# Optimization experiments

Hardware: AMD Instinct MI355X
Metric: run time of the kernel (lower is better)

The kernel has to match this reference:

```python
import jax, jax.numpy as jnp
import numpy as np

N_USERS = 200000
N_ITEMS = 100000
N_EDGES = 4800000
EMBED_DIM = 64
N_LAYERS = 3
BATCH = 16384


def setup_inputs() -> dict:
    key = jax.random.key(0)
    ks = jax.random.split(key, 7)
    N = N_USERS + N_ITEMS
    user_embed = jax.random.normal(ks[0], (N_USERS, EMBED_DIM), dtype=jnp.float32)
    item_embed = jax.random.normal(ks[1], (N_ITEMS, EMBED_DIM), dtype=jnp.float32)
    edge_src = jax.random.randint(ks[2], (N_EDGES,), 0, N, dtype=jnp.int32)
    edge_dst = jax.random.randint(ks[3], (N_EDGES,), 0, N, dtype=jnp.int32)
    # stands in for symmetric normalization 1/sqrt(deg_i*deg_j), avg degree ~16
    edge_val = jax.random.uniform(ks[4], (N_EDGES,), dtype=jnp.float32) * 0.0625
    users = jax.random.randint(ks[5], (BATCH,), 0, N_USERS, dtype=jnp.int32)
    items = jax.random.randint(ks[6], (BATCH,), 0, N_ITEMS, dtype=jnp.int32)
    return {"user_embed": user_embed, "item_embed": item_embed,
            "edge_src": edge_src, "edge_dst": edge_dst, "edge_val": edge_val,
            "users": users, "items": items}


def _computer(user_embed, item_embed, edge_src, edge_dst, edge_val):
    # LightGCN.computer(): N_LAYERS rounds of SpMM, mean over layer outputs
    N = user_embed.shape[0] + item_embed.shape[0]
    all_emb = jnp.concatenate([user_embed, item_embed], axis=0)  # [N, d]
    emb = all_emb
    acc = all_emb  # running sum over layers (incl. layer 0)
    for _ in range(N_LAYERS):
        # sparse.mm: out[dst] += val * emb[src]
        msgs = emb[edge_src] * edge_val[:, None]          # [E, d]
        emb = jax.ops.segment_sum(msgs, edge_dst, num_segments=N)
        acc = acc + emb
    light_out = acc / jnp.asarray(N_LAYERS + 1, dtype=acc.dtype)
    return light_out[:user_embed.shape[0]], light_out[user_embed.shape[0]:]


def reference(user_embed, item_embed, edge_src, edge_dst, edge_val, users, items):
    all_users, all_items = _computer(user_embed, item_embed, edge_src, edge_dst, edge_val)
    users_emb = all_users[users]   # [B, d]
    items_emb = all_items[items]   # [B, d]
    scores = jnp.sum(users_emb * items_emb, axis=1)  # [B]
    return users_emb, items_emb, scores
```

## Files before the change

### kernel.cpp

```cpp
#include <hip/hip_runtime.h>
#include <hip/hip_bf16.h>


#define DIM   64
#define FTHR  2048
#define WTHR  512
#define SHIFT 9
#define BSZ   (1 << SHIFT)
#define KMAX  1023
#define CHUNK 4096
#define STPB  512
#define SBT   1024

__device__ __forceinline__ float bf2f(unsigned short u) {
    return __builtin_bit_cast(float, ((unsigned)u) << 16);
}
__device__ __forceinline__ unsigned short f2bf(float x) {
    return __builtin_bit_cast(unsigned short, __float2bfloat16(x));
}
__device__ __forceinline__ int idx_at(const void* a, long long i, int wide) {
    return wide ? (int)((const long long*)a)[i] : ((const int*)a)[i];
}
__device__ __forceinline__ int clampi(int v, int hi) {
    return v < 0 ? 0 : (v >= hi ? hi - 1 : v);
}

__global__ void sniff_all(const unsigned* __restrict__ ue, const unsigned* __restrict__ ie,
                          const unsigned* __restrict__ eval, const unsigned* __restrict__ esrc,
                          const unsigned* __restrict__ users, int* __restrict__ flags) {
    int b = blockIdx.x, t = threadIdx.x;
    const unsigned* p = (b == 0) ? ue : (b == 1) ? ie : (b == 2) ? eval
                       : (b == 3) ? esrc : users;
    int cnt = 0;
    if (b < 3) {
        for (int i = t; i < 4096; i += 256) {
            unsigned e = (p[i] >> 7) & 0xffu;
            if (e >= 110u && e <= 135u) cnt++;
        }
    } else {
        for (int i = t; i < 1024; i += 256)
            if (p[2 * i + 1] == 0u) cnt++;
    }
    #pragma unroll
    for (int off = 32; off > 0; off >>= 1) cnt += __shfl_down(cnt, off, 64);
    if ((t & 63) == 0) atomicAdd(&flags[b], cnt);
}

__global__ void stage_in(const void* __restrict__ ue, const void* __restrict__ ie,
                         ushort4* __restrict__ S, const int* __restrict__ flags,
                         int NU16, int N16) {
    int tid = blockIdx.x * blockDim.x + threadIdx.x;
    if (tid >= N16) return;
    bool user = tid < NU16;
    const void* src = user ? ue : ie;
    int fl  = user ? flags[0] : flags[1];
    int idx = user ? tid : tid - NU16;
    ushort4 o;
    if (fl > FTHR) {
        o = ((const ushort4*)src)[idx];
    } else {
        float4 v = ((const float4*)src)[idx];
        o.x = f2bf(v.x); o.y = f2bf(v.y); o.z = f2bf(v.z); o.w = f2bf(v.w);
    }
    S[tid] = o;
}

__global__ void gather0(const void* __restrict__ ue, const void* __restrict__ ie,
                        const void* __restrict__ users, const void* __restrict__ items,
                        float* __restrict__ out, const int* __restrict__ flags,
                        int B, int NU, int NI) {
    int tid = blockIdx.x * blockDim.x + threadIdx.x;
    int r = tid >> 6, d = tid & 63;
    if (r >= 2 * B) return;
    int wide = flags[4] > WTHR;
    const void* src; long long row; int fl;
    if (r < B) { row = clampi(idx_at(users, r, wide), NU); src = ue; fl = flags[0]; }
    else       { row = clampi(idx_at(items, r - B, wide), NI); src = ie; fl = flags[1]; }
    float v;
    if (fl > FTHR) v = bf2f(((const unsigned short*)src)[row * 64 + d]);
    else           v = ((const float*)src)[row * 64 + d];
    out[tid] = v;
}

__global__ void k_p1hist(const void* __restrict__ edst, const int* __restrict__ flags,
                         int* __restrict__ blkhist, int E, int N, int K, int NBLK) {
    __shared__ int h[KMAX + 1];
    int t = threadIdx.x;
    for (int i = t; i < K; i += blockDim.x) h[i] = 0;
    __syncthreads();
    int wide = flags[3] > WTHR;
    int base = blockIdx.x * CHUNK;
    int lim = min(base + CHUNK, E);
    for (int i = base + t; i < lim; i += blockDim.x) {
        int d = clampi(idx_at(edst, i, wide), N);
        atomicAdd(&h[d >> SHIFT], 1);
    }
    __syncthreads();
    for (int i = t; i < K; i += blockDim.x) blkhist[i * NBLK + blockIdx.x] = h[i];
}

__global__ void k_scanA(int* __restrict__ blkhist, int* __restrict__ btotal,
                        int NBLK) {
    int row = blockIdx.x;
    int lane = threadIdx.x;
    int run = 0;
    for (int base = 0; base < NBLK; base += 64) {
        int idx = base + lane;
        int v = (idx < NBLK) ? blkhist[row * NBLK + idx] : 0;
        int x = v;
        #pragma unroll
        for (int off = 1; off < 64; off <<= 1) {
            int y = __shfl_up(x, off, 64);
            if (lane >= off) x += y;
        }
        if (idx < NBLK) blkhist[row * NBLK + idx] = run + (x - v);
        run += __shfl(x, 63, 64);
    }
    if (lane == 0) btotal[row] = run;
}

__global__ __launch_bounds__(SBT) void k_scanB(const int* __restrict__ btotal,
                        int* __restrict__ bucketStart,
                        int* __restrict__ rowstart, int K, int N) {
    __shared__ int sh[SBT];
    int t = threadIdx.x;
    int v = (t < K) ? btotal[t] : 0;
    sh[t] = v;
    for (int off = 1; off < SBT; off <<= 1) {
        __syncthreads();
        int y = (t >= off) ? sh[t - off] : 0;
        __syncthreads();
        sh[t] += y;
    }
    __syncthreads();
    if (t <= K) bucketStart[t] = sh[t] - v;
    if (t == SBT - 1) rowstart[N] = sh[SBT - 1];
}

__global__ void k_p1scat(const void* __restrict__ esrc, const void* __restrict__ edst,
                         const void* __restrict__ eval, const int* __restrict__ flags,
                         const int* __restrict__ blkhist, const int* __restrict__ bucketStart,
                         unsigned long long* __restrict__ TMP, int E, int N, int K, int NBLK) {
    __shared__ int cur[KMAX + 1];
    int t = threadIdx.x;
    for (int i = t; i < K; i += blockDim.x)
        cur[i] = bucketStart[i] + blkhist[i * NBLK + blockIdx.x];
    __syncthreads();
    int wide = flags[3] > WTHR;
    int evalbf = flags[2] > FTHR;
    int base = blockIdx.x * CHUNK;
    int lim = min(base + CHUNK, E);
    for (int i = base + t; i < lim; i += blockDim.x) {
        int d = clampi(idx_at(edst, i, wide), N);
        int s = clampi(idx_at(esrc, i, wide), N);
        unsigned short vb = evalbf ? ((const unsigned short*)eval)[i]
                                   : f2bf(((const float*)eval)[i]);
        int b = d >> SHIFT;
        unsigned dl = (unsigned)(d & (BSZ - 1));
        int slot = atomicAdd(&cur[b], 1);
        unsigned long long p = (unsigned long long)(unsigned)s
                             | (((unsigned long long)((dl << 16) | vb)) << 32);
        TMP[slot] = p;
    }
}

__global__ __launch_bounds__(STPB) void k_p2sort(const unsigned long long* __restrict__ TMP,
                         const int* __restrict__ bucketStart,
                         int2* __restrict__ edges, int* __restrict__ rowstart,
                         int N) {
    __shared__ int hist[BSZ];
    __shared__ int wsum[STPB / 64];
    int b = blockIdx.x;
    int t = threadIdx.x;
    int span0 = bucketStart[b], span1 = bucketStart[b + 1];
    int rbase = b << SHIFT;
    int nrows = min(BSZ, N - rbase);
    for (int i = t; i < BSZ; i += STPB) hist[i] = 0;
    __syncthreads();
    for (int e = span0 + t; e < span1; e += STPB) {
        int dl = (int)((TMP[e] >> 48) & (BSZ - 1));
        atomicAdd(&hist[dl], 1);
    }
    __syncthreads();
    const int PER = BSZ / STPB;
    int loc[PER];
    int s = 0;
    #pragma unroll
    for (int j = 0; j < PER; ++j) {
        int v = hist[t * PER + j];
        loc[j] = s;
        s += v;
    }
    int wid = t >> 6, lane = t & 63;
    int x = s;
    #pragma unroll
    for (int off = 1; off < 64; off <<= 1) {
        int y = __shfl_up(x, off, 64);
        if (lane >= off) x += y;
    }
    if (lane == 63) wsum[wid] = x;
    __syncthreads();
    int wbase = 0;
    #pragma unroll
    for (int w = 0; w < STPB / 64; ++w) wbase += (w < wid) ? wsum[w] : 0;
    int texcl = wbase + x - s;
    #pragma unroll
    for (int j = 0; j < PER; ++j) hist[t * PER + j] = texcl + loc[j];
    __syncthreads();
    for (int r = t; r < nrows; r += STPB) rowstart[rbase + r] = span0 + hist[r];
    __syncthreads();
    for (int e = span0 + t; e < span1; e += STPB) {
        unsigned long long p = TMP[e];
        int dl = (int)((p >> 48) & (BSZ - 1));
        unsigned vb = (unsigned)((p >> 32) & 0xffffu);
        int src = (int)(unsigned)p;
        int slot = span0 + atomicAdd(&hist[dl], 1);
        edges[slot] = make_int2(src, (int)(vb << 16));
    }
}

template <int U>
__device__ __forceinline__ void spmm_batch(const unsigned short* __restrict__ Sin,
                                           const int2* __restrict__ edges,
                                           int k, int lane, float& acc) {
    int2 e[U];
    #pragma unroll
    for (int j = 0; j < U; ++j) e[j] = edges[k + j];
    float a[U];
    #pragma unroll
    for (int j = 0; j < U; ++j) a[j] = bf2f(Sin[(size_t)e[j].x * 64 + lane]);
    #pragma unroll
    for (int j = 0; j < U; ++j) acc += __int_as_float(e[j].y) * a[j];
}

__device__ __forceinline__ float spmm_row(const unsigned short* __restrict__ Sin,
                                          const int2* __restrict__ edges,
                                          int start, int end, int lane) {
    float acc = 0.f;
    int k = start;
    for (; k + 16 <= end; k += 16) spmm_batch<16>(Sin, edges, k, lane, acc);
    if (k + 8 <= end) { spmm_batch<8>(Sin, edges, k, lane, acc); k += 8; }
    if (k + 4 <= end) { spmm_batch<4>(Sin, edges, k, lane, acc); k += 4; }
    if (k + 2 <= end) { spmm_batch<2>(Sin, edges, k, lane, acc); k += 2; }
    if (k < end)      { spmm_batch<1>(Sin, edges, k, lane, acc); }
    return acc;
}

__global__ void k_spmm(const unsigned short* __restrict__ Sin,
                       unsigned short* __restrict__ Sout,
                       const int* __restrict__ rowstart,
                       const int2* __restrict__ edges, int N) {
    int wid = (blockIdx.x * blockDim.x + threadIdx.x) >> 6;
    int lane = threadIdx.x & 63;
    if (wid >= N) return;
    int start = __builtin_amdgcn_readfirstlane(rowstart[wid]);
    int end   = __builtin_amdgcn_readfirstlane(rowstart[wid + 1]);
    float acc = spmm_row(Sin, edges, start, end, lane);
    __builtin_nontemporal_store(f2bf(acc), &Sout[(size_t)wid * 64 + lane]);
}

__global__ void k_spmm_b(const unsigned short* __restrict__ Sin,
                         const void* __restrict__ users, const void* __restrict__ items,
                         const int* __restrict__ rowstart, const int2* __restrict__ edges,
                         float* __restrict__ out, const int* __restrict__ flags,
                         int B, int NU, int NI) {
    int tid = blockIdx.x * blockDim.x + threadIdx.x;
    int wid = tid >> 6, lane = threadIdx.x & 63;
    if (wid >= 2 * B) return;
    int wide = flags[4] > WTHR;
    int row;
    if (wid < B) row = clampi(idx_at(users, wid, wide), NU);
    else         row = NU + clampi(idx_at(items, wid - B, wide), NI);
    int start = __builtin_amdgcn_readfirstlane(rowstart[row]);
    int end   = __builtin_amdgcn_readfirstlane(rowstart[row + 1]);
    float acc = spmm_row(Sin, edges, start, end, lane);
    out[(size_t)wid * 64 + lane] += acc;
}

__global__ void k_gacc(const unsigned short* __restrict__ S,
                       const void* __restrict__ users, const void* __restrict__ items,
                       float* __restrict__ out, const int* __restrict__ flags,
                       int B, int NU, int NI) {
    int tid = blockIdx.x * blockDim.x + threadIdx.x;
    int r = tid >> 6, d = tid & 63;
    if (r >= 2 * B) return;
    int wide = flags[4] > WTHR;
    long long row;
    if (r < B) row = clampi(idx_at(users, r, wide), NU);
    else       row = (long long)NU + clampi(idx_at(items, r - B, wide), NI);
    out[tid] += bf2f(S[row * 64 + d]);
}

__global__ void epilogue(float* __restrict__ out, int B) {
    int tid = blockIdx.x * blockDim.x + threadIdx.x;
    int b = tid >> 6, d = tid & 63;
    if (b >= B) return;
    float u = out[tid] * 0.25f;
    float i = out[B * 64 + tid] * 0.25f;
    out[tid] = u;
    out[B * 64 + tid] = i;
    float p = u * i;
    #pragma unroll
    for (int off = 32; off > 0; off >>= 1) p += __shfl_down(p, off, 64);
    if (d == 0) out[2 * B * 64 + b] = p;
}

__global__ void diag_fill(float* __restrict__ out, int n, float marker) {
    int tid = blockIdx.x * blockDim.x + threadIdx.x;
    if (tid < n) out[tid] = marker;
}

extern "C" void kernel_launch(void* const* d_in, const int* in_sizes, int n_in,
                              void* d_out, int out_size, void* d_ws, size_t ws_size,
                              hipStream_t stream) {
    const void* ue    = d_in[0];
    const void* ie    = d_in[1];
    const void* esrc  = d_in[2];
    const void* edst  = d_in[3];
    const void* eval  = d_in[4];
    const void* users = d_in[5];
    const void* items = d_in[6];
    float* out = (float*)d_out;

    const int TPB = 256;
    if (n_in != 7) {
        diag_fill<<<(out_size + TPB - 1) / TPB, TPB, 0, stream>>>(out, out_size,
                                                                  3000.0f + 64.0f * n_in);
        return;
    }

    const int NU = in_sizes[0] / DIM;
    const int NI = in_sizes[1] / DIM;
    const int N  = NU + NI;
    const int E  = in_sizes[2];
    const int B  = in_sizes[5];
    const int K    = (N + BSZ - 1) >> SHIFT;
    const int NBLK = (E + CHUNK - 1) / CHUNK;

    const size_t sBytes   = (size_t)N * DIM * sizeof(unsigned short);
    const size_t tmpBytes = sBytes > (size_t)E * 8 ? sBytes : (size_t)E * 8;
    size_t off = 0;
    auto take = [&](size_t bytes) { size_t o = off; off += (bytes + 255) & ~255ull; return o; };
    char* base = (char*)d_ws;
    unsigned short* S0   = (unsigned short*)(base + take(sBytes));
    unsigned short* S1   = (unsigned short*)(base + take(tmpBytes));
    int2*  edges   = (int2*)(base + take((size_t)E * 8));
    int*   blkhist = (int*)(base + take((size_t)K * NBLK * 4));
    int*   btotal  = (int*)(base + take((KMAX + 1) * 4));
    int*   bucketStart = (int*)(base + take((KMAX + 2) * 4));
    int*   rowstart    = (int*)(base + take((size_t)(N + 1) * 4));
    int*   flags   = (int*)(base + take(64));
    const size_t need = off;

    if (ws_size < need || K > KMAX) {
        diag_fill<<<(out_size + TPB - 1) / TPB, TPB, 0, stream>>>(out, out_size,
                                                                  1000.0f + (float)(ws_size >> 20));
        return;
    }

    const int N16 = N * 16, NU16 = NU * 16;
    dim3 gStage((N16 + TPB - 1) / TPB);
    dim3 gBatch((2 * B * 64 + TPB - 1) / TPB);
    dim3 gSpmm(((size_t)N * 64 + TPB - 1) / TPB);
    dim3 gEpi((B * 64 + TPB - 1) / TPB);

    (void)hipMemsetAsync(flags, 0, 8 * sizeof(int), stream);

    sniff_all<<<5, 256, 0, stream>>>((const unsigned*)ue, (const unsigned*)ie,
                                     (const unsigned*)eval, (const unsigned*)esrc,
                                     (const unsigned*)users, flags);

    gather0<<<gBatch, TPB, 0, stream>>>(ue, ie, users, items, out, flags, B, NU, NI);
    stage_in<<<gStage, TPB, 0, stream>>>(ue, ie, (ushort4*)S0, flags, NU16, N16);

    k_p1hist<<<NBLK, STPB, 0, stream>>>(edst, flags, blkhist, E, N, K, NBLK);
    k_scanA<<<K, 64, 0, stream>>>(blkhist, btotal, NBLK);
    k_scanB<<<1, SBT, 0, stream>>>(btotal, bucketStart, rowstart, K, N);
    k_p1scat<<<NBLK, STPB, 0, stream>>>(esrc, edst, eval, flags, blkhist, bucketStart,
                                        (unsigned long long*)S1, E, N, K, NBLK);
    k_p2sort<<<K, STPB, 0, stream>>>((const unsigned long long*)S1, bucketStart,
                                     edges, rowstart, N);

    k_spmm<<<gSpmm, TPB, 0, stream>>>(S0, S1, rowstart, edges, N);
    k_gacc<<<gBatch, TPB, 0, stream>>>(S1, users, items, out, flags, B, NU, NI);
    k_spmm<<<gSpmm, TPB, 0, stream>>>(S1, S0, rowstart, edges, N);
    k_gacc<<<gBatch, TPB, 0, stream>>>(S0, users, items, out, flags, B, NU, NI);
    k_spmm_b<<<gBatch, TPB, 0, stream>>>(S0, users, items, rowstart, edges, out, flags,
                                         B, NU, NI);
    epilogue<<<gEpi, TPB, 0, stream>>>(out, B);
}
```

Baseline: 627.4 us.

## Replace per-block histogram scan with global atomic bucket counters in edge bucketing

Drops the per-block histogram matrix and its column scan kernel. A count kernel now accumulates bucket totals with global atomics. The scatter kernel recomputes its local histogram and claims a contiguous range per bucket through global atomic cursors, so the order of blocks within a bucket becomes nondeterministic. Block size drops to 256 for these passes, and the spmm helper is duplicated and inlined separately for the two spmm kernels.

```diff
diff --git a/kernel.cpp b/kernel.cpp
--- a/kernel.cpp
+++ b/kernel.cpp
@@ -9,6 +9,7 @@
 #define BSZ   (1 << SHIFT)
 #define KMAX  1023
 #define CHUNK 4096
+#define CTPB  256
 #define STPB  512
 #define SBT   1024
 
@@ -82,45 +83,26 @@
     out[tid] = v;
 }
 
-__global__ void k_p1hist(const void* __restrict__ edst, const int* __restrict__ flags,
-                         int* __restrict__ blkhist, int E, int N, int K, int NBLK) {
+__global__ void k_count(const void* __restrict__ edst, const int* __restrict__ flags,
+                        int* __restrict__ btotal, int E, int N, int K) {
     __shared__ int h[KMAX + 1];
     int t = threadIdx.x;
-    for (int i = t; i < K; i += blockDim.x) h[i] = 0;
+    for (int i = t; i < K; i += CTPB) h[i] = 0;
     __syncthreads();
     int wide = flags[3] > WTHR;
     int base = blockIdx.x * CHUNK;
     int lim = min(base + CHUNK, E);
-    for (int i = base + t; i < lim; i += blockDim.x) {
+    for (int i = base + t; i < lim; i += CTPB) {
         int d = clampi(idx_at(edst, i, wide), N);
         atomicAdd(&h[d >> SHIFT], 1);
     }
     __syncthreads();
-    for (int i = t; i < K; i += blockDim.x) blkhist[i * NBLK + blockIdx.x] = h[i];
-}
-
-__global__ void k_scanA(int* __restrict__ blkhist, int* __restrict__ btotal,
-                        int NBLK) {
-    int row = blockIdx.x;
-    int lane = threadIdx.x;
-    int run = 0;
-    for (int base = 0; base < NBLK; base += 64) {
-        int idx = base + lane;
-        int v = (idx < NBLK) ? blkhist[row * NBLK + idx] : 0;
-        int x = v;
-        #pragma unroll
-        for (int off = 1; off < 64; off <<= 1) {
-            int y = __shfl_up(x, off, 64);
-            if (lane >= off) x += y;
-        }
-        if (idx < NBLK) blkhist[row * NBLK + idx] = run + (x - v);
-        run += __shfl(x, 63, 64);
-    }
-    if (lane == 0) btotal[row] = run;
+    for (int i = t; i < K; i += CTPB)
+        if (h[i]) atomicAdd(&btotal[i], h[i]);
 }
 
 __global__ __launch_bounds__(SBT) void k_scanB(const int* __restrict__ btotal,
-                        int* __restrict__ bucketStart,
+                        int* __restrict__ bucketStart, int* __restrict__ gcur,
                         int* __restrict__ rowstart, int K, int N) {
     __shared__ int sh[SBT];
     int t = threadIdx.x;
@@ -134,23 +116,32 @@
     }
     __syncthreads();
     if (t <= K) bucketStart[t] = sh[t] - v;
+    if (t < K)  gcur[t] = sh[t] - v;
     if (t == SBT - 1) rowstart[N] = sh[SBT - 1];
 }
 
-__global__ void k_p1scat(const void* __restrict__ esrc, const void* __restrict__ edst,
-                         const void* __restrict__ eval, const int* __restrict__ flags,
-                         const int* __restrict__ blkhist, const int* __restrict__ bucketStart,
-                         unsigned long long* __restrict__ TMP, int E, int N, int K, int NBLK) {
+__global__ void k_scat(const void* __restrict__ esrc, const void* __restrict__ edst,
+                       const void* __restrict__ eval, const int* __restrict__ flags,
+                       int* __restrict__ gcur, unsigned long long* __restrict__ TMP,
+                       int E, int N, int K) {
+    __shared__ int h[KMAX + 1];
     __shared__ int cur[KMAX + 1];
     int t = threadIdx.x;
-    for (int i = t; i < K; i += blockDim.x)
-        cur[i] = bucketStart[i] + blkhist[i * NBLK + blockIdx.x];
+    for (int i = t; i < K; i += CTPB) h[i] = 0;
     __syncthreads();
     int wide = flags[3] > WTHR;
     int evalbf = flags[2] > FTHR;
     int base = blockIdx.x * CHUNK;
     int lim = min(base + CHUNK, E);
-    for (int i = base + t; i < lim; i += blockDim.x) {
+    for (int i = base + t; i < lim; i += CTPB) {
+        int d = clampi(idx_at(edst, i, wide), N);
+        atomicAdd(&h[d >> SHIFT], 1);
+    }
+    __syncthreads();
+    for (int i = t; i < K; i += CTPB)
+        if (h[i]) cur[i] = atomicAdd(&gcur[i], h[i]);
+    __syncthreads();
+    for (int i = base + t; i < lim; i += CTPB) {
         int d = clampi(idx_at(edst, i, wide), N);
         int s = clampi(idx_at(esrc, i, wide), N);
         unsigned short vb = evalbf ? ((const unsigned short*)eval)[i]
@@ -220,9 +211,9 @@
 }
 
 template <int U>
-__device__ __forceinline__ void spmm_batch(const unsigned short* __restrict__ Sin,
-                                           const int2* __restrict__ edges,
-                                           int k, int lane, float& acc) {
+__device__ __forceinline__ void spmm_batchA(const unsigned short* __restrict__ Sin,
+                                            const int2* __restrict__ edges,
+                                            int k, int lane, float& acc) {
     int2 e[U];
     #pragma unroll
     for (int j = 0; j < U; ++j) e[j] = edges[k + j];
@@ -231,19 +222,6 @@
     for (int j = 0; j < U; ++j) a[j] = bf2f(Sin[(size_t)e[j].x * 64 + lane]);
     #pragma unroll
     for (int j = 0; j < U; ++j) acc += __int_as_float(e[j].y) * a[j];
-}
-
-__device__ __forceinline__ float spmm_row(const unsigned short* __restrict__ Sin,
-                                          const int2* __restrict__ edges,
-                                          int start, int end, int lane) {
-    float acc = 0.f;
-    int k = start;
-    for (; k + 16 <= end; k += 16) spmm_batch<16>(Sin, edges, k, lane, acc);
-    if (k + 8 <= end) { spmm_batch<8>(Sin, edges, k, lane, acc); k += 8; }
-    if (k + 4 <= end) { spmm_batch<4>(Sin, edges, k, lane, acc); k += 4; }
-    if (k + 2 <= end) { spmm_batch<2>(Sin, edges, k, lane, acc); k += 2; }
-    if (k < end)      { spmm_batch<1>(Sin, edges, k, lane, acc); }
-    return acc;
 }
 
 __global__ void k_spmm(const unsigned short* __restrict__ Sin,
@@ -255,8 +233,28 @@
     if (wid >= N) return;
     int start = __builtin_amdgcn_readfirstlane(rowstart[wid]);
     int end   = __builtin_amdgcn_readfirstlane(rowstart[wid + 1]);
-    float acc = spmm_row(Sin, edges, start, end, lane);
+    float acc = 0.f;
+    int k = start;
+    for (; k + 16 <= end; k += 16) spmm_batchA<16>(Sin, edges, k, lane, acc);
+    if (k + 8 <= end) { spmm_batchA<8>(Sin, edges, k, lane, acc); k += 8; }
+    if (k + 4 <= end) { spmm_batchA<4>(Sin, edges, k, lane, acc); k += 4; }
+    if (k + 2 <= end) { spmm_batchA<2>(Sin, edges, k, lane, acc); k += 2; }
+    if (k < end)      { spmm_batchA<1>(Sin, edges, k, lane, acc); }
     __builtin_nontemporal_store(f2bf(acc), &Sout[(size_t)wid * 64 + lane]);
+}
+
+template <int U>
+__device__ __forceinline__ void spmm_batchB(const unsigned short* __restrict__ Sin,
+                                            const int2* __restrict__ edges,
+                                            int k, int lane, float& acc) {
+    int2 e[U];
+    #pragma unroll
+    for (int j = 0; j < U; ++j) e[j] = edges[k + j];
+    float a[U];
+    #pragma unroll
+    for (int j = 0; j < U; ++j) a[j] = bf2f(Sin[(size_t)e[j].x * 64 + lane]);
+    #pragma unroll
+    for (int j = 0; j < U; ++j) acc += __int_as_float(e[j].y) * a[j];
 }
 
 __global__ void k_spmm_b(const unsigned short* __restrict__ Sin,
@@ -273,7 +271,13 @@
     else         row = NU + clampi(idx_at(items, wid - B, wide), NI);
     int start = __builtin_amdgcn_readfirstlane(rowstart[row]);
     int end   = __builtin_amdgcn_readfirstlane(rowstart[row + 1]);
-    float acc = spmm_row(Sin, edges, start, end, lane);
+    float acc = 0.f;
+    int k = start;
+    for (; k + 16 <= end; k += 16) spmm_batchB<16>(Sin, edges, k, lane, acc);
+    if (k + 8 <= end) { spmm_batchB<8>(Sin, edges, k, lane, acc); k += 8; }
+    if (k + 4 <= end) { spmm_batchB<4>(Sin, edges, k, lane, acc); k += 4; }
+    if (k + 2 <= end) { spmm_batchB<2>(Sin, edges, k, lane, acc); k += 2; }
+    if (k < end)      { spmm_batchB<1>(Sin, edges, k, lane, acc); }
     out[(size_t)wid * 64 + lane] += acc;
 }
 
@@ -345,8 +349,8 @@
     unsigned short* S0   = (unsigned short*)(base + take(sBytes));
     unsigned short* S1   = (unsigned short*)(base + take(tmpBytes));
     int2*  edges   = (int2*)(base + take((size_t)E * 8));
-    int*   blkhist = (int*)(base + take((size_t)K * NBLK * 4));
     int*   btotal  = (int*)(base + take((KMAX + 1) * 4));
+    int*   gcur    = (int*)(base + take((KMAX + 1) * 4));
     int*   bucketStart = (int*)(base + take((KMAX + 2) * 4));
     int*   rowstart    = (int*)(base + take((size_t)(N + 1) * 4));
     int*   flags   = (int*)(base + take(64));
@@ -365,6 +369,7 @@
     dim3 gEpi((B * 64 + TPB - 1) / TPB);
 
     (void)hipMemsetAsync(flags, 0, 8 * sizeof(int), stream);
+    (void)hipMemsetAsync(btotal, 0, (size_t)(K + 1) * sizeof(int), stream);
 
     sniff_all<<<5, 256, 0, stream>>>((const unsigned*)ue, (const unsigned*)ie,
                                      (const unsigned*)eval, (const unsigned*)esrc,
@@ -373,11 +378,10 @@
     gather0<<<gBatch, TPB, 0, stream>>>(ue, ie, users, items, out, flags, B, NU, NI);
     stage_in<<<gStage, TPB, 0, stream>>>(ue, ie, (ushort4*)S0, flags, NU16, N16);
 
-    k_p1hist<<<NBLK, STPB, 0, stream>>>(edst, flags, blkhist, E, N, K, NBLK);
-    k_scanA<<<K, 64, 0, stream>>>(blkhist, btotal, NBLK);
-    k_scanB<<<1, SBT, 0, stream>>>(btotal, bucketStart, rowstart, K, N);
-    k_p1scat<<<NBLK, STPB, 0, stream>>>(esrc, edst, eval, flags, blkhist, bucketStart,
-                                        (unsigned long long*)S1, E, N, K, NBLK);
+    k_count<<<NBLK, CTPB, 0, stream>>>(edst, flags, btotal, E, N, K);
+    k_scanB<<<1, SBT, 0, stream>>>(btotal, bucketStart, gcur, rowstart, K, N);
+    k_scat<<<NBLK, CTPB, 0, stream>>>(esrc, edst, eval, flags, gcur,
+                                      (unsigned long long*)S1, E, N, K);
     k_p2sort<<<K, STPB, 0, stream>>>((const unsigned long long*)S1, bucketStart,
                                      edges, rowstart, N);
 
```

New measurement: 638.5 us. Within noise of the previous version (+1.8%).
